# Kernel optimization log

Measured on AMD Instinct MI355X. Metric: run time of the kernel, lower is better.

## Reference

```python
import jax, jax.numpy as jnp
import numpy as np

E = 2  # expand_ratio


def _linear_scan(u, a):
    """h_t = a_t * h_{t-1} + u_t along axis 0, h_{-1}=0. Parallel associative scan."""
    def comb(x, y):
        a1, b1 = x
        a2, b2 = y
        return a2 * a1, a2 * b1 + b2
    _, h = jax.lax.associative_scan(comb, (a, u), axis=0)
    return h


def setup_inputs() -> dict:
    key = jax.random.key(0)
    ks = jax.random.split(key, 8)
    n, b, d = 2048, 4, 1024
    s = 1.0 / np.sqrt(d)
    return {
        "x": jax.random.normal(ks[0], (n, b, d), jnp.float32),
        "lower_bound": jax.random.uniform(ks[1], (d,), jnp.float32),
        "W_in": jax.random.normal(ks[2], (d, 3 * d), jnp.float32) * s,
        "b_in": jnp.zeros((3 * d,), jnp.float32),
        "W_out": jax.random.normal(ks[3], (d, d), jnp.float32) * s,
        "b_out": jnp.zeros((d,), jnp.float32),
        "gamma": jnp.ones((d,), jnp.float32),
        "beta": jnp.zeros((d,), jnp.float32),
    }


def reference(x, lower_bound, W_in, b_in, W_out, b_out, gamma, beta):
    n, b, d = x.shape
    h = d // E
    feat = x @ W_in + b_in                      # (n,b,3d)
    inp, og, fg = jnp.split(feat, 3, axis=-1)
    inp = jax.nn.silu(inp)
    og = jax.nn.sigmoid(og)
    fg = jax.nn.sigmoid(fg)
    # reshape (h d) -> h, d=E
    inp = inp.reshape(n, b, h, E)
    og = og.reshape(n, b, h, E)
    fg = fg.reshape(n, b, h, E)
    lb = lower_bound.reshape(h, E)
    lam = lb + (1.0 - lb) * fg                  # (n,b,h,E)
    # outer-product input: (1-lam) outer inp over the E dims -> (n,b,h,E,E)
    u = jnp.einsum('nbhd,nbhe->nbhde', 1.0 - lam, inp)
    a = jnp.broadcast_to(lam[..., None], u.shape)
    u = u.reshape(n, b, h * E * E)
    a = a.reshape(n, b, h * E * E)
    state_fwd = _linear_scan(u, a)
    state_rev = jnp.flip(_linear_scan(jnp.flip(u, 0), jnp.flip(a, 0)), 0)
    state = (state_fwd + state_rev).reshape(n, b, h, E, E)
    out = jnp.einsum('nbhde,nbhd->nbhe', state, og).reshape(n, b, d)
    # layernorm over last dim
    mu = jnp.mean(out, axis=-1, keepdims=True)
    var = jnp.var(out, axis=-1, keepdims=True)
    out = (out - mu) * jax.lax.rsqrt(var + 1e-5) * gamma + beta
    return out @ W_out + b_out
```

## Files before the change

### kernel.cpp

```cpp
#include <hip/hip_runtime.h>

typedef __bf16 bf16x8 __attribute__((ext_vector_type(8)));
typedef float floatx4 __attribute__((ext_vector_type(4)));

#define NCH 128
#define CLEN 16

__device__ __forceinline__ unsigned short f2bf(float f) {
  unsigned int u = __builtin_bit_cast(unsigned int, f);
  u += 0x7fff + ((u >> 16) & 1);
  return (unsigned short)(u >> 16);
}
__device__ __forceinline__ float bf2f(unsigned short u) {
  unsigned int v = (unsigned int)u << 16;
  return __builtin_bit_cast(float, v);
}
__device__ __forceinline__ float bf2f_lo(unsigned int u) {
  return __builtin_bit_cast(float, u << 16);
}
__device__ __forceinline__ float bf2f_hi(unsigned int u) {
  return __builtin_bit_cast(float, u & 0xffff0000u);
}

__device__ __forceinline__ void async_copy16(const void* g, void* l) {
  __builtin_amdgcn_global_load_lds(
      (const __attribute__((address_space(1))) unsigned int*)g,
      (__attribute__((address_space(3))) unsigned int*)l, 16, 0, 0);
}

__global__ void cast_x_kernel(const float* __restrict__ in, unsigned short* __restrict__ out) {
  int i = blockIdx.x * blockDim.x + threadIdx.x;
  float4 v = ((const float4*)in)[i];
  ushort4 o;
  o.x = f2bf(v.x); o.y = f2bf(v.y); o.z = f2bf(v.z); o.w = f2bf(v.w);
  ((ushort4*)out)[i] = o;
}

__global__ void tcast2_kernel(const float* __restrict__ Win, unsigned short* __restrict__ winT,
                              const float* __restrict__ Wout, unsigned short* __restrict__ woutT) {
  __shared__ float tile[32][33];
  int bx = blockIdx.x;
  const float* W;
  unsigned short* WT;
  int ncols, n0;
  if (bx < 96) { W = Win; WT = winT; ncols = 3072; n0 = bx * 32; }
  else { W = Wout; WT = woutT; ncols = 1024; n0 = (bx - 96) * 32; }
  int k0 = blockIdx.y * 32;
  int tx = threadIdx.x, ty = threadIdx.y;
  tile[ty][tx] = W[(size_t)(k0 + ty) * ncols + n0 + tx];
  __syncthreads();
  WT[(size_t)(n0 + ty) * 1024 + k0 + tx] = f2bf(tile[tx][ty]);
}

template <int EPI>
__global__ __launch_bounds__(256) void gemm_kernel(
    const unsigned short* __restrict__ A, const unsigned short* __restrict__ BT,
    const float* __restrict__ bias, const float* __restrict__ lb,
    float* __restrict__ outf,
    unsigned short* __restrict__ o_inp, unsigned short* __restrict__ o_og,
    unsigned short* __restrict__ o_om) {
  __shared__ alignas(16) char smem_raw[17408];
  unsigned short* As = (unsigned short*)smem_raw;
  unsigned short* Bs = As + 128 * 32;
  const int m0 = blockIdx.x * 128, n0 = blockIdx.y * 128;
  const int tid = threadIdx.x;
  const int lane = tid & 63, wave = tid >> 6;
  const int wm = (wave >> 1) * 64, wn = (wave & 1) * 64;
  const int mrow = lane & 15, q = lane >> 4;
  const int qsw = q ^ ((mrow >> 1) & 3);
  floatx4 acc[4][4] = {};
  const int r0 = wave * 32;
  const int srow = r0 + (lane >> 2);
  const int qs = (lane & 3) ^ ((srow >> 1) & 3);
  const unsigned short* gA0 = A + (size_t)(m0 + srow) * 1024 + qs * 8;
  const unsigned short* gA1 = gA0 + (size_t)16 * 1024;
  const unsigned short* gB0 = BT + (size_t)(n0 + srow) * 1024 + qs * 8;
  const unsigned short* gB1 = gB0 + (size_t)16 * 1024;
  unsigned short* lA0 = &As[r0 * 32];
  unsigned short* lA1 = &As[(r0 + 16) * 32];
  unsigned short* lB0 = &Bs[r0 * 32];
  unsigned short* lB1 = &Bs[(r0 + 16) * 32];
  for (int kt = 0; kt < 1024; kt += 32) {
    __syncthreads();
    async_copy16(gA0, lA0);
    async_copy16(gA1, lA1);
    async_copy16(gB0, lB0);
    async_copy16(gB1, lB1);
    gA0 += 32; gA1 += 32; gB0 += 32; gB1 += 32;
    __syncthreads();
    bf16x8 af[4], bf[4];
#pragma unroll
    for (int i = 0; i < 4; i++) af[i] = *(const bf16x8*)&As[(wm + i * 16 + mrow) * 32 + qsw * 8];
#pragma unroll
    for (int j = 0; j < 4; j++) bf[j] = *(const bf16x8*)&Bs[(wn + j * 16 + mrow) * 32 + qsw * 8];
#pragma unroll
    for (int i = 0; i < 4; i++)
#pragma unroll
      for (int j = 0; j < 4; j++)
        acc[i][j] = __builtin_amdgcn_mfma_f32_16x16x32_bf16(af[i], bf[j], acc[i][j], 0, 0, 0);
  }
  const int er = tid >> 3;
  const int ec = (tid & 7) * 16;
  const int rgbase = m0 + (er & 15) + (er >> 4) * 64;
  const int lr = (wm ? 16 : 0) + q * 4;
  float bi[4];
  int cidx[4];
#pragma unroll
  for (int j = 0; j < 4; j++) {
    cidx[j] = n0 + wn + j * 16 + mrow;
    bi[j] = bias[cidx[j]];
  }
  if (EPI == 1) {
    unsigned short* Cs = (unsigned short*)smem_raw;
    const int seg = n0 >> 10;
    unsigned short* dst = (seg == 0) ? o_inp : (seg == 1) ? o_og : o_om;
    float Lv[4];
    if (seg == 2) {
#pragma unroll
      for (int j = 0; j < 4; j++) Lv[j] = lb[cidx[j] & 1023];
    }
#pragma unroll
    for (int i = 0; i < 4; i++) {
      __syncthreads();
#pragma unroll
      for (int j = 0; j < 4; j++) {
        const int lc = wn + j * 16 + mrow;
#pragma unroll
        for (int g = 0; g < 4; g++) {
          float v = acc[i][j][g] + bi[j];
          unsigned short ob;
          if (seg == 0) { float s = 1.f / (1.f + __expf(-v)); ob = f2bf(v * s); }
          else if (seg == 1) { float s = 1.f / (1.f + __expf(-v)); ob = f2bf(s); }
          else { float sm = 1.f / (1.f + __expf(v)); ob = f2bf((1.f - Lv[j]) * sm); }
          Cs[(lr + g) * 136 + lc] = ob;
        }
      }
      __syncthreads();
      uint4 v0 = *(uint4*)&Cs[er * 136 + ec];
      uint4 v1 = *(uint4*)&Cs[er * 136 + ec + 8];
      size_t ro = (size_t)(rgbase + i * 16) * 1024 + (n0 & 1023) + ec;
      *(uint4*)&dst[ro] = v0;
      *(uint4*)&dst[ro + 8] = v1;
    }
  } else {
    float* Cf = (float*)smem_raw;
#pragma unroll
    for (int i = 0; i < 4; i++) {
      __syncthreads();
#pragma unroll
      for (int j = 0; j < 4; j++) {
        const int lc = wn + j * 16 + mrow;
#pragma unroll
        for (int g = 0; g < 4; g++) Cf[(lr + g) * 132 + lc] = acc[i][j][g] + bi[j];
      }
      __syncthreads();
      size_t ro = (size_t)(rgbase + i * 16) * 1024 + n0 + ec;
#pragma unroll
      for (int k = 0; k < 4; k++) {
        float4 v = *(float4*)&Cf[er * 132 + ec + k * 4];
        *(float4*)&outf[ro + k * 4] = v;
      }
    }
  }
}

__global__ void scan_passA(const unsigned short* __restrict__ om, const unsigned short* __restrict__ ip,
                           float* __restrict__ sumA, float* __restrict__ sumBf,
                           float* __restrict__ sumBr) {
  int idx = blockIdx.x * 256 + threadIdx.x;
  int h = idx & 511, cb = idx >> 9, b = cb & 3, c = cb >> 2;
  long base = ((long)c * CLEN * 4 + b) * 1024 + 2 * h;
  float p0 = 1.f, p1 = 1.f;
  float s00 = 0.f, s01 = 0.f, s10 = 0.f, s11 = 0.f;
  float r00 = 0.f, r01 = 0.f, r10 = 0.f, r11 = 0.f;
#pragma unroll
  for (int t = 0; t < CLEN; t++) {
    ushort2 l2 = *(const ushort2*)(om + base);
    ushort2 i2 = *(const ushort2*)(ip + base);
    base += 4096;
    float omx = bf2f(l2.x), omy = bf2f(l2.y);
    float ipx = bf2f(i2.x), ipy = bf2f(i2.y);
    float lx = 1.f - omx, ly = 1.f - omy;
    float u00 = omx * ipx, u01 = omx * ipy, u10 = omy * ipx, u11 = omy * ipy;
    r00 += p0 * u00; r01 += p0 * u01; r10 += p1 * u10; r11 += p1 * u11;
    s00 = lx * s00 + u00; s01 = lx * s01 + u01;
    s10 = ly * s10 + u10; s11 = ly * s11 + u11;
    p0 *= lx; p1 *= ly;
  }
  ((float2*)sumA)[idx] = make_float2(p0, p1);
  ((float4*)sumBf)[idx] = make_float4(s00, s01, s10, s11);
  ((float4*)sumBr)[idx] = make_float4(r00, r01, r10, r11);
}

__global__ void scan_passB(const float* __restrict__ sumA, const float* __restrict__ sumBf,
                           const float* __restrict__ sumBr, float* __restrict__ initF,
                           float* __restrict__ initR) {
  int tid = blockIdx.x * 256 + threadIdx.x;
  int dir = tid >> 13;
  int rem = tid & 8191;
  int ch = rem & 3;
  int bh = rem >> 2;
  int dd = ch >> 1;
  if (dir == 0) {
    float H = 0.f;
    for (int c = 0; c < NCH; c++) {
      int si = c * 2048 + bh;
      initF[(size_t)si * 4 + ch] = H;
      H = sumA[(size_t)si * 2 + dd] * H + sumBf[(size_t)si * 4 + ch];
    }
  } else {
    float G = 0.f;
    for (int c = NCH - 1; c >= 0; c--) {
      int si = c * 2048 + bh;
      initR[(size_t)si * 4 + ch] = G;
      G = sumA[(size_t)si * 2 + dd] * G + sumBr[(size_t)si * 4 + ch];
    }
  }
}

__global__ __launch_bounds__(512) void scanC_ln_kernel(
    const unsigned short* __restrict__ om, const unsigned short* __restrict__ ip,
    const unsigned short* __restrict__ og,
    const float* __restrict__ initF, const float* __restrict__ initR,
    const float* __restrict__ gamma, const float* __restrict__ beta,
    unsigned short* __restrict__ ybf) {
  __shared__ float tile[8][1024];
  __shared__ float ldsG[1024];
  __shared__ float ldsB[1024];
  const int h = threadIdx.x;
  const int cb = blockIdx.x;
  const int b = cb & 3, c = cb >> 2;
  const int idx = cb * 512 + h;
  *(float2*)&ldsG[2 * h] = *(const float2*)(gamma + 2 * h);
  *(float2*)&ldsB[2 * h] = *(const float2*)(beta + 2 * h);
  float4 F = ((const float4*)initF)[idx];
  float4 R = ((const float4*)initR)[idx];
  float outx[CLEN], outy[CLEN];
  unsigned int lS[CLEN], iS[CLEN], oS[CLEN];
  const long base = ((long)c * CLEN * 4 + b) * 1024 + 2 * h;
  float h00 = F.x, h01 = F.y, h10 = F.z, h11 = F.w;
  long p = base;
#pragma unroll
  for (int t = 0; t < CLEN; t++) {
    unsigned int l2 = *(const unsigned int*)(om + p);
    unsigned int i2 = *(const unsigned int*)(ip + p);
    unsigned int o2 = *(const unsigned int*)(og + p);
    p += 4096;
    lS[t] = l2; iS[t] = i2; oS[t] = o2;
    float omx = bf2f_lo(l2), omy = bf2f_hi(l2);
    float ipx = bf2f_lo(i2), ipy = bf2f_hi(i2);
    float ox = bf2f_lo(o2), oy = bf2f_hi(o2);
    float lx = 1.f - omx, ly = 1.f - omy;
    h00 = lx * h00 + omx * ipx; h01 = lx * h01 + omx * ipy;
    h10 = ly * h10 + omy * ipx; h11 = ly * h11 + omy * ipy;
    outx[t] = h00 * ox + h10 * oy;
    outy[t] = h01 * ox + h11 * oy;
  }
  float g00 = R.x, g01 = R.y, g10 = R.z, g11 = R.w;
#pragma unroll
  for (int t = CLEN - 1; t >= 0; t--) {
    unsigned int l2 = lS[t], i2 = iS[t], o2 = oS[t];
    float omx = bf2f_lo(l2), omy = bf2f_hi(l2);
    float ipx = bf2f_lo(i2), ipy = bf2f_hi(i2);
    float ox = bf2f_lo(o2), oy = bf2f_hi(o2);
    float lx = 1.f - omx, ly = 1.f - omy;
    g00 = omx * ipx + lx * g00; g01 = omx * ipy + lx * g01;
    g10 = omy * ipx + ly * g10; g11 = omy * ipy + ly * g11;
    outx[t] += g00 * ox + g10 * oy;
    outy[t] += g01 * ox + g11 * oy;
  }
  const int lane = h & 63, wv = h >> 6;
#pragma unroll
  for (int g = 0; g < CLEN / 8; g++) {
    __syncthreads();
#pragma unroll
    for (int r = 0; r < 8; r++) {
      float2 v2 = make_float2(outx[g * 8 + r], outy[g * 8 + r]);
      *(float2*)&tile[r][2 * h] = v2;
    }
    __syncthreads();
    {
      const int t = g * 8 + wv;
      float4 v[4];
#pragma unroll
      for (int k = 0; k < 4; k++) v[k] = *(const float4*)&tile[wv][lane * 16 + k * 4];
      float s = 0.f, s2 = 0.f;
#pragma unroll
      for (int k = 0; k < 4; k++) {
        s += v[k].x + v[k].y + v[k].z + v[k].w;
        s2 += v[k].x * v[k].x + v[k].y * v[k].y + v[k].z * v[k].z + v[k].w * v[k].w;
      }
#pragma unroll
      for (int off = 1; off < 64; off <<= 1) {
        s += __shfl_xor(s, off);
        s2 += __shfl_xor(s2, off);
      }
      float mean = s * (1.f / 1024.f);
      float var = s2 * (1.f / 1024.f) - mean * mean;
      float rstd = rsqrtf(var + 1e-5f);
      unsigned short o16[16];
#pragma unroll
      for (int k = 0; k < 4; k++) {
        float* vv = (float*)&v[k];
#pragma unroll
        for (int e = 0; e < 4; e++) {
          int ch = lane * 16 + k * 4 + e;
          o16[k * 4 + e] = f2bf((vv[e] - mean) * rstd * ldsG[ch] + ldsB[ch]);
        }
      }
      size_t rowo = ((size_t)(c * CLEN + t) * 4 + b) * 1024 + lane * 16;
      *(uint4*)(ybf + rowo) = *(uint4*)&o16[0];
      *(uint4*)(ybf + rowo + 8) = *(uint4*)&o16[8];
    }
  }
}

extern "C" void kernel_launch(void* const* d_in, const int* in_sizes, int n_in,
                              void* d_out, int out_size, void* d_ws, size_t ws_size,
                              hipStream_t stream) {
  const float* x = (const float*)d_in[0];
  const float* lb = (const float*)d_in[1];
  const float* Win = (const float*)d_in[2];
  const float* bin = (const float*)d_in[3];
  const float* Wout = (const float*)d_in[4];
  const float* bout = (const float*)d_in[5];
  const float* gamma = (const float*)d_in[6];
  const float* beta = (const float*)d_in[7];
  float* out = (float*)d_out;

  char* ws = (char*)d_ws;
  size_t off = 0;
  auto alloc = [&](size_t bytes) {
    void* p = ws + off;
    off += (bytes + 255) & ~(size_t)255;
    return p;
  };
  unsigned short* x_bf = (unsigned short*)alloc(8192ull * 1024 * 2);
  unsigned short* winT = (unsigned short*)alloc(3072ull * 1024 * 2);
  unsigned short* woutT = (unsigned short*)alloc(1024ull * 1024 * 2);
  unsigned short* inp_b = (unsigned short*)alloc(8192ull * 1024 * 2);
  unsigned short* og_b = (unsigned short*)alloc(8192ull * 1024 * 2);
  unsigned short* om_b = (unsigned short*)alloc(8192ull * 1024 * 2);
  unsigned short* y_bf = (unsigned short*)alloc(8192ull * 1024 * 2);
  float* sumA = (float*)alloc((size_t)NCH * 4 * 512 * 2 * 4);
  float* sumBf = (float*)alloc((size_t)NCH * 4 * 512 * 4 * 4);
  float* sumBr = (float*)alloc((size_t)NCH * 4 * 512 * 4 * 4);
  float* initF = (float*)alloc((size_t)NCH * 4 * 512 * 4 * 4);
  float* initR = (float*)alloc((size_t)NCH * 4 * 512 * 4 * 4);

  cast_x_kernel<<<8192, 256, 0, stream>>>(x, x_bf);
  tcast2_kernel<<<dim3(128, 32), dim3(32, 32), 0, stream>>>(Win, winT, Wout, woutT);
  gemm_kernel<1><<<dim3(64, 24), 256, 0, stream>>>(x_bf, winT, bin, lb, nullptr, inp_b, og_b, om_b);
  scan_passA<<<(NCH * 4 * 512) / 256, 256, 0, stream>>>(om_b, inp_b, sumA, sumBf, sumBr);
  scan_passB<<<64, 256, 0, stream>>>(sumA, sumBf, sumBr, initF, initR);
  scanC_ln_kernel<<<NCH * 4, 512, 0, stream>>>(om_b, inp_b, og_b, initF, initR, gamma, beta, y_bf);
  gemm_kernel<0><<<dim3(64, 8), 256, 0, stream>>>(y_bf, woutT, bout, nullptr, out, nullptr, nullptr, nullptr);
}
```

Measured before the change: 246.2 us.

## Replace input-projection GEMM with 256x256-tile, 8-wave pipelined MFMA kernel

Adds a dedicated GEMM kernel for the input projection. It uses 256x256 output tiles, 512 threads and a 128KB LDS double buffer. Async global-to-LDS copies are interleaved with MFMA sub-steps under explicit barriers and wave priority raises. It also uses XOR-swizzled LDS layouts and a remapped block order for L2 locality. The goal is better data reuse and latency hiding than the generic templated GEMM, at the cost of high register and LDS pressure and a brittle hand-scheduled sync pattern.

```diff
diff --git a/kernel.cpp b/kernel.cpp
--- a/kernel.cpp
+++ b/kernel.cpp
@@ -164,6 +164,199 @@
   }
 }
 
+__global__ __launch_bounds__(512, 2) void gemm1_kernel(
+    const unsigned short* __restrict__ A, const unsigned short* __restrict__ BT,
+    const float* __restrict__ bias, const float* __restrict__ lb,
+    unsigned short* __restrict__ o_inp, unsigned short* __restrict__ o_og,
+    unsigned short* __restrict__ o_om) {
+  __shared__ alignas(16) char smem[131072];
+  const int orig = blockIdx.x;
+  const int wg = (orig & 7) * 48 + (orig >> 3);
+  const int m0 = (wg & 31) << 8;
+  const int n0 = (wg >> 5) << 8;
+  const int tid = threadIdx.x;
+  const int lane = tid & 63, wave = tid >> 6;
+  const int wm = wave >> 2, wn = wave & 3;
+  const int srow = tid >> 3;
+  const int sq = (tid & 7) ^ (srow & 7);
+  const unsigned short* gA = A + (size_t)(m0 + srow) * 1024 + sq * 8;
+  const unsigned short* gB = BT + (size_t)(n0 + srow) * 1024 + sq * 8;
+  char* lw = smem + wave * 1024;
+  const int aro = (wm * 128 + (lane & 15)) * 128;
+  const int bro = (wn * 64 + (lane & 15)) * 128;
+  const int qs0 = ((lane >> 4) ^ (lane & 7)) * 16;
+  const int qs1 = ((4 + (lane >> 4)) ^ (lane & 7)) * 16;
+
+  floatx4 acc[8][4] = {};
+  bf16x8 aF[4][2], bF[4][2];
+
+#define STG(lofs, gh, kk)                                \
+  do {                                                   \
+    const unsigned short* _g = (gh) + (size_t)(kk) * 64; \
+    async_copy16(_g, lw + (lofs));                       \
+    async_copy16(_g + 65536, lw + (lofs) + 8192);        \
+  } while (0)
+#define RA(base, mh, i, s) \
+  (*(const bf16x8*)(smem + (base) + aro + (mh) * 8192 + (i) * 2048 + ((s) ? qs1 : qs0)))
+#define RB(base, j, s) \
+  (*(const bf16x8*)(smem + (base) + bro + (j) * 2048 + ((s) ? qs1 : qs0)))
+#define BAR __builtin_amdgcn_s_barrier()
+#define LGKM0 asm volatile("s_waitcnt lgkmcnt(0)" ::: "memory")
+#define VM4 asm volatile("s_waitcnt vmcnt(4)" ::: "memory")
+#define MM(d, a, b) d = __builtin_amdgcn_mfma_f32_16x16x32_bf16(a, b, d, 0, 0, 0)
+
+  STG(65536, gB, 0);
+  STG(65536 + 16384, gB + 131072, 0);
+  STG(0, gA, 0);
+  STG(0 + 16384, gA + 131072, 0);
+  STG(98304, gB, 1);
+  STG(98304 + 16384, gB + 131072, 1);
+  VM4;
+  BAR;
+
+#pragma unroll 1
+  for (int it = 0; it < 8; ++it) {
+    const int t0 = 2 * it;
+    const int kA1 = t0 + 1;
+    const int kN2 = (t0 + 2 > 15) ? 15 : t0 + 2;
+    const int kN3 = (t0 + 3 > 15) ? 15 : t0 + 3;
+#pragma unroll
+    for (int i = 0; i < 4; i++) { aF[i][0] = RA(0, 0, i, 0); aF[i][1] = RA(0, 0, i, 1); }
+#pragma unroll
+    for (int j = 0; j < 2; j++) { bF[j][0] = RB(65536, j, 0); bF[j][1] = RB(65536, j, 1); }
+    STG(32768, gA, kA1);
+    BAR; LGKM0;
+    __builtin_amdgcn_s_setprio(1);
+#pragma unroll
+    for (int i = 0; i < 4; i++)
+#pragma unroll
+      for (int j = 0; j < 2; j++) { MM(acc[i][j], aF[i][0], bF[j][0]); MM(acc[i][j], aF[i][1], bF[j][1]); }
+    __builtin_amdgcn_s_setprio(0);
+    BAR;
+#pragma unroll
+    for (int j = 2; j < 4; j++) { bF[j][0] = RB(65536, j, 0); bF[j][1] = RB(65536, j, 1); }
+    STG(32768 + 16384, gA + 131072, kA1);
+    BAR; LGKM0;
+    __builtin_amdgcn_s_setprio(1);
+#pragma unroll
+    for (int i = 0; i < 4; i++)
+#pragma unroll
+      for (int j = 2; j < 4; j++) { MM(acc[i][j], aF[i][0], bF[j][0]); MM(acc[i][j], aF[i][1], bF[j][1]); }
+    __builtin_amdgcn_s_setprio(0);
+    BAR;
+#pragma unroll
+    for (int i = 0; i < 4; i++) { aF[i][0] = RA(0, 1, i, 0); aF[i][1] = RA(0, 1, i, 1); }
+    STG(65536, gB, kN2);
+    BAR; LGKM0;
+    __builtin_amdgcn_s_setprio(1);
+#pragma unroll
+    for (int i = 0; i < 4; i++)
+#pragma unroll
+      for (int j = 0; j < 2; j++) { MM(acc[4 + i][j], aF[i][0], bF[j][0]); MM(acc[4 + i][j], aF[i][1], bF[j][1]); }
+    __builtin_amdgcn_s_setprio(0);
+    BAR;
+    STG(65536 + 16384, gB + 131072, kN2);
+    BAR;
+    __builtin_amdgcn_s_setprio(1);
+#pragma unroll
+    for (int i = 0; i < 4; i++)
+#pragma unroll
+      for (int j = 2; j < 4; j++) { MM(acc[4 + i][j], aF[i][0], bF[j][0]); MM(acc[4 + i][j], aF[i][1], bF[j][1]); }
+    __builtin_amdgcn_s_setprio(0);
+    VM4;
+    BAR;
+#pragma unroll
+    for (int i = 0; i < 4; i++) { aF[i][0] = RA(32768, 0, i, 0); aF[i][1] = RA(32768, 0, i, 1); }
+#pragma unroll
+    for (int j = 0; j < 2; j++) { bF[j][0] = RB(98304, j, 0); bF[j][1] = RB(98304, j, 1); }
+    STG(0, gA, kN2);
+    BAR; LGKM0;
+    __builtin_amdgcn_s_setprio(1);
+#pragma unroll
+    for (int i = 0; i < 4; i++)
+#pragma unroll
+      for (int j = 0; j < 2; j++) { MM(acc[i][j], aF[i][0], bF[j][0]); MM(acc[i][j], aF[i][1], bF[j][1]); }
+    __builtin_amdgcn_s_setprio(0);
+    BAR;
+#pragma unroll
+    for (int j = 2; j < 4; j++) { bF[j][0] = RB(98304, j, 0); bF[j][1] = RB(98304, j, 1); }
+    STG(16384, gA + 131072, kN2);
+    BAR; LGKM0;
+    __builtin_amdgcn_s_setprio(1);
+#pragma unroll
+    for (int i = 0; i < 4; i++)
+#pragma unroll
+      for (int j = 2; j < 4; j++) { MM(acc[i][j], aF[i][0], bF[j][0]); MM(acc[i][j], aF[i][1], bF[j][1]); }
+    __builtin_amdgcn_s_setprio(0);
+    BAR;
+#pragma unroll
+    for (int i = 0; i < 4; i++) { aF[i][0] = RA(32768, 1, i, 0); aF[i][1] = RA(32768, 1, i, 1); }
+    STG(98304, gB, kN3);
+    BAR; LGKM0;
+    __builtin_amdgcn_s_setprio(1);
+#pragma unroll
+    for (int i = 0; i < 4; i++)
+#pragma unroll
+      for (int j = 0; j < 2; j++) { MM(acc[4 + i][j], aF[i][0], bF[j][0]); MM(acc[4 + i][j], aF[i][1], bF[j][1]); }
+    __builtin_amdgcn_s_setprio(0);
+    BAR;
+    STG(98304 + 16384, gB + 131072, kN3);
+    BAR;
+    __builtin_amdgcn_s_setprio(1);
+#pragma unroll
+    for (int i = 0; i < 4; i++)
+#pragma unroll
+      for (int j = 2; j < 4; j++) { MM(acc[4 + i][j], aF[i][0], bF[j][0]); MM(acc[4 + i][j], aF[i][1], bF[j][1]); }
+    __builtin_amdgcn_s_setprio(0);
+    VM4;
+    BAR;
+  }
+#undef STG
+#undef RA
+#undef RB
+#undef BAR
+#undef LGKM0
+#undef VM4
+#undef MM
+
+  asm volatile("s_waitcnt vmcnt(0) lgkmcnt(0)" ::: "memory");
+  const int seg = n0 >> 10;
+  unsigned short* dst = (seg == 0) ? o_inp : (seg == 1) ? o_og : o_om;
+  unsigned short* Cs = (unsigned short*)smem;
+  float bi[4], Lv[4];
+#pragma unroll
+  for (int j = 0; j < 4; j++) {
+    const int c = n0 + wn * 64 + j * 16 + (lane & 15);
+    bi[j] = bias[c];
+    Lv[j] = (seg == 2) ? lb[c & 1023] : 0.f;
+  }
+  const int lrw = wm * 16 + (lane >> 4) * 4;
+  const int lcw = wn * 64 + (lane & 15);
+  const int er = tid >> 4, ec = (tid & 15) * 16;
+  const int growb = m0 + (er >> 4) * 128 + (er & 15);
+#pragma unroll
+  for (int i = 0; i < 8; i++) {
+    __syncthreads();
+#pragma unroll
+    for (int j = 0; j < 4; j++)
+#pragma unroll
+      for (int g = 0; g < 4; g++) {
+        float v = acc[i][j][g] + bi[j];
+        unsigned short ob;
+        if (seg == 0) { float s = 1.f / (1.f + __expf(-v)); ob = f2bf(v * s); }
+        else if (seg == 1) { float s = 1.f / (1.f + __expf(-v)); ob = f2bf(s); }
+        else { float sm = 1.f / (1.f + __expf(v)); ob = f2bf((1.f - Lv[j]) * sm); }
+        Cs[(lrw + g) * 264 + lcw + j * 16] = ob;
+      }
+    __syncthreads();
+    uint4 v0 = *(uint4*)&Cs[er * 264 + ec];
+    uint4 v1 = *(uint4*)&Cs[er * 264 + ec + 8];
+    size_t ro = (size_t)(growb + i * 16) * 1024 + (n0 & 1023) + ec;
+    *(uint4*)&dst[ro] = v0;
+    *(uint4*)&dst[ro + 8] = v1;
+  }
+}
+
 __global__ void scan_passA(const unsigned short* __restrict__ om, const unsigned short* __restrict__ ip,
                            float* __restrict__ sumA, float* __restrict__ sumBf,
                            float* __restrict__ sumBr) {
@@ -350,7 +543,7 @@
 
   cast_x_kernel<<<8192, 256, 0, stream>>>(x, x_bf);
   tcast2_kernel<<<dim3(128, 32), dim3(32, 32), 0, stream>>>(Win, winT, Wout, woutT);
-  gemm_kernel<1><<<dim3(64, 24), 256, 0, stream>>>(x_bf, winT, bin, lb, nullptr, inp_b, og_b, om_b);
+  gemm1_kernel<<<384, 512, 0, stream>>>(x_bf, winT, bin, lb, inp_b, og_b, om_b);
   scan_passA<<<(NCH * 4 * 512) / 256, 256, 0, stream>>>(om_b, inp_b, sumA, sumBf, sumBr);
   scan_passB<<<64, 256, 0, stream>>>(sumA, sumBf, sumBr, initF, initR);
   scanC_ln_kernel<<<NCH * 4, 512, 0, stream>>>(om_b, inp_b, og_b, initF, initR, gamma, beta, y_bf);
```

Result: slower. 258.6 us (+5.0%).
